# Optimization experiments

Measured on AMD Instinct MI355X. Metric: run time of the kernel, lower is better.

Reference implementation:

```python
import jax, jax.numpy as jnp
from jax import lax
import numpy as np


def setup_inputs() -> dict:
    key = jax.random.key(0)
    T, W = 2048, 30  # document length, max span width
    starts = jnp.repeat(jnp.arange(T, dtype=jnp.int32), W)      # [T*W]
    widths = jnp.tile(jnp.arange(W, dtype=jnp.int32), T)        # [T*W]
    ends = jnp.minimum(starts + widths, T - 1)
    spans = jnp.stack([starts, ends], axis=1)                   # [N,2], N=61440
    N = spans.shape[0]
    scores = jax.random.normal(key, (N,), dtype=jnp.float32)
    mask = jnp.ones((N,), dtype=jnp.float32)
    return {
        "spans": spans,
        "span_mention_scores": scores,
        "span_mask": mask,
        "token_num": T,
        "num_spans_to_keep": int(0.4 * T),
    }


def _greedy_non_crossing(spans, scores, mask, T, k):
    """Greedy NMS-style selection of up to k spans with no crossing overlap.
    Faithful to masked_topk_non_overlap: iterate candidates in descending
    (score + log(mask)) order; a candidate (s,e) is rejected iff it crosses
    an already-selected span, tracked via start_to_max_end / end_to_min_start
    tables. Sequential dependence expressed as lax.scan; the O(span_width)
    inner token loop is vectorized as an O(T) masked range query.
    """
    N = scores.shape[0]
    order = jnp.argsort(-(scores + jnp.log(mask)))  # descending sort
    starts = spans[:, 0].astype(jnp.int32)
    ends = spans[:, 1].astype(jnp.int32)
    tok = jnp.arange(T, dtype=jnp.int32)

    def step(carry, c):
        s2e, e2s, sel, cnt = carry
        s = starts[c]
        e = ends[c]
        # token_idx in (s, e] with start_to_max_end[token_idx] > e -> crossing
        cross1 = jnp.any((tok > s) & (tok <= e) & (s2e > e))
        # token_idx in [s, e) with 0 <= end_to_min_start[token_idx] < s -> crossing
        cross2 = jnp.any((tok >= s) & (tok < e) & (e2s >= 0) & (e2s < s))
        accept = jnp.logical_and(jnp.logical_not(cross1 | cross2), cnt < k)
        # start_to_max_end[s] = max(old, e) if accepted
        s2e = s2e.at[s].set(jnp.where(accept, jnp.maximum(s2e[s], e), s2e[s]))
        # end_to_min_start[e] = s if unset or s smaller, if accepted
        cur = e2s[e]
        e2s = e2s.at[e].set(jnp.where(accept & ((cur == -1) | (s < cur)), s, cur))
        sel = sel.at[c].set(sel[c] | accept)
        cnt = cnt + accept.astype(jnp.int32)
        return (s2e, e2s, sel, cnt), None

    init = (jnp.full((T,), -1, dtype=jnp.int32),
            jnp.full((T,), -1, dtype=jnp.int32),
            jnp.zeros((N,), dtype=bool),
            jnp.int32(0))
    (s2e, e2s, sel, cnt), _ = lax.scan(step, init, order)

    # sort selected candidates by (start, end); pad to fixed size k
    sort_key = jnp.where(sel, starts * T + ends, T * T)  # T*T > any valid key
    idx = jnp.argsort(sort_key)[:k]
    valid = jnp.arange(k) < cnt
    top_idx = jnp.where(valid, idx, 0)
    return top_idx, valid


def reference(spans, span_mention_scores, span_mask, token_num, num_spans_to_keep):
    top_idx, valid = _greedy_non_crossing(
        spans, span_mention_scores, span_mask, token_num, num_spans_to_keep)
    top_scores = jnp.where(valid, span_mention_scores[top_idx], 0.0)
    top_spans = jnp.where(valid[:, None], spans[top_idx], 0)
    return top_scores, top_idx, top_spans, valid
```

## Files before the change

kernel.cpp:

```cpp
#include <hip/hip_runtime.h>
#include <math.h>
#include <limits.h>

#define TPB   1024
#define TILE  1024
#define MAXT  2048
#define TPAD  64
#define MAXK  1024
#define MAXW  29
#define BATCH 1024
#define FLAGSTRIDE 16

struct SortSM {
  union {
    unsigned h[4 * 256];
    unsigned wcnt[16][256];
  };
  unsigned baseL[256];
};

__device__ inline void dbar(unsigned* flg, int nblk) {
  __syncthreads();
  if (threadIdx.x == 0) {
    __threadfence();
    atomicExch(&flg[blockIdx.x * FLAGSTRIDE], 1u);
  }
  if ((int)threadIdx.x < nblk) {
    int spin = 0;
    while (__hip_atomic_load(&flg[threadIdx.x * FLAGSTRIDE], __ATOMIC_ACQUIRE,
                             __HIP_MEMORY_SCOPE_AGENT) == 0u) {
      __builtin_amdgcn_s_sleep(2);
      if ((++spin & 255) == 0) {
        if (atomicAdd(&flg[threadIdx.x * FLAGSTRIDE], 0u) != 0u) break;
      }
    }
  }
  __syncthreads();
  if (threadIdx.x == 0) __threadfence();
  __syncthreads();
}

__device__ inline bool precheck30(const unsigned* tabP, int cc, int cs, int ce) {
  if (cc < 0) return false;
  int w = ce - cs;
  bool crossed = false;
  #pragma unroll
  for (int off = 0; off <= MAXW; ++off) {
    unsigned tv = tabP[cs + off];
    crossed |= ((off >= 1) & (off <= w) & ((tv & 0xFFFFu) > (unsigned)(ce + 1)))
             | ((off < w) & ((tv >> 16) < (unsigned)cs));
  }
  for (int off = MAXW + 1; off <= w; ++off) {
    unsigned tv = tabP[cs + off];
    crossed |= ((tv & 0xFFFFu) > (unsigned)(ce + 1));
    if (off < w) crossed |= ((tv >> 16) < (unsigned)cs);
  }
  return !crossed;
}

__global__ void __launch_bounds__(TPB, 4) fused_kernel(
    const int* __restrict__ spans, const float* __restrict__ scores,
    const float* __restrict__ mask, const int* __restrict__ tnum_p,
    const int* __restrict__ keep_p, float* __restrict__ out, int N, int nT,
    unsigned* pflag, unsigned* ghist, unsigned* tileCnt,
    unsigned* keysA, unsigned* keysB, int* idxA, int* idxB) {
  const int2* spans2 = (const int2*)spans;
  __shared__ SortSM s;
  __shared__ unsigned base4[4][256];
  const int tid = threadIdx.x;
  const int lane = tid & 63;
  const int wave = tid >> 6;

  if (tid < 1024) s.h[tid] = 0;
  __syncthreads();
  {
    int i = blockIdx.x * TILE + tid;
    if (i < N) {
      float kf = scores[i] + logf(mask[i]);
      unsigned u = __float_as_uint(kf);
      u = (u & 0x80000000u) ? ~u : (u | 0x80000000u);
      u = ~u;
      keysA[i] = u;
      atomicAdd(&s.h[(u & 255u)], 1u);
      atomicAdd(&s.h[256 + ((u >> 8) & 255u)], 1u);
      atomicAdd(&s.h[512 + ((u >> 16) & 255u)], 1u);
      atomicAdd(&s.h[768 + (u >> 24)], 1u);
    }
    __syncthreads();
    if (tid < 1024 && s.h[tid]) atomicAdd(&ghist[tid], s.h[tid]);
  }
  dbar(pflag + 0 * nT * FLAGSTRIDE, nT);

  if (wave < 4) {
    const int p = wave;
    unsigned v0 = ghist[p * 256 + 4 * lane + 0];
    unsigned v1 = ghist[p * 256 + 4 * lane + 1];
    unsigned v2 = ghist[p * 256 + 4 * lane + 2];
    unsigned v3 = ghist[p * 256 + 4 * lane + 3];
    unsigned sum = v0 + v1 + v2 + v3;
    unsigned x = sum;
    for (int off = 1; off < 64; off <<= 1) {
      unsigned y = __shfl_up(x, off, 64);
      if (lane >= off) x += y;
    }
    unsigned excl = x - sum;
    base4[p][4 * lane + 0] = excl;
    base4[p][4 * lane + 1] = excl + v0;
    base4[p][4 * lane + 2] = excl + v0 + v1;
    base4[p][4 * lane + 3] = excl + v0 + v1 + v2;
  }
  __syncthreads();

  for (int p = 0; p < 4; ++p) {
    const unsigned* srck = (p & 1) ? keysB : keysA;
    const int*      srci = (p & 1) ? idxB : idxA;
    unsigned*       dstk = (p & 1) ? keysA : keysB;
    int*            dsti = (p & 1) ? idxA : idxB;
    const int shift = 8 * p;
    unsigned* lbf = pflag + (1 + p) * nT * FLAGSTRIDE;

    for (int j = tid; j < 16 * 256; j += TPB)
      (&s.wcnt[0][0])[j] = 0;
    __syncthreads();

    int i = blockIdx.x * TILE + tid;
    bool v = (i < N);
    unsigned key = v ? srck[i] : 0u;
    int pay = v ? ((p == 0) ? i : srci[i]) : 0;
    unsigned d = (key >> shift) & 255u;
    unsigned long long mm = __ballot(v);
    #pragma unroll
    for (int b = 0; b < 8; ++b) {
      unsigned long long bb = __ballot((d >> b) & 1u);
      mm &= ((d >> b) & 1u) ? bb : ~bb;
    }
    unsigned rnk = (unsigned)__popcll(mm & ((1ull << lane) - 1ull));
    if (v && rnk == 0) s.wcnt[wave][d] = (unsigned)__popcll(mm);
    __syncthreads();
    if (tid < 256) {
      unsigned run = 0;
      #pragma unroll
      for (int g = 0; g < 16; ++g) {
        unsigned c = s.wcnt[g][tid];
        s.wcnt[g][tid] = run;
        run += c;
      }
      tileCnt[blockIdx.x * 256 + tid] = run;
    }
    __syncthreads();

    if (tid == 0) {
      __threadfence();
      atomicExch(&lbf[blockIdx.x * FLAGSTRIDE], 1u);
    }
    if (tid < blockIdx.x) {
      int spin = 0;
      while (__hip_atomic_load(&lbf[tid * FLAGSTRIDE], __ATOMIC_ACQUIRE,
                               __HIP_MEMORY_SCOPE_AGENT) == 0u) {
        __builtin_amdgcn_s_sleep(2);
        if ((++spin & 255) == 0) {
          if (atomicAdd(&lbf[tid * FLAGSTRIDE], 0u) != 0u) break;
        }
      }
    }
    __syncthreads();
    if (tid == 0) __threadfence();
    __syncthreads();

    if (tid < 256) {
      unsigned baseacc = base4[p][tid];
      for (int t = 0; t < blockIdx.x; ++t)
        baseacc += tileCnt[t * 256 + tid];
      s.baseL[tid] = baseacc;
    }
    __syncthreads();
    if (v) {
      unsigned pos = s.baseL[d] + s.wcnt[wave][d] + rnk;
      dstk[pos] = key;
      dsti[pos] = pay;
    }
    if (p < 3) {
      dbar(pflag + (5 + p) * nT * FLAGSTRIDE, nT);
    }
  }

  {
    unsigned* fin = pflag + 8 * nT * FLAGSTRIDE;
    __syncthreads();
    if (tid == 0) {
      __threadfence();
      atomicExch(&fin[blockIdx.x * FLAGSTRIDE], 1u);
    }
    if (blockIdx.x != 0) return;
    if (tid < nT) {
      int spin = 0;
      while (__hip_atomic_load(&fin[tid * FLAGSTRIDE], __ATOMIC_ACQUIRE,
                               __HIP_MEMORY_SCOPE_AGENT) == 0u) {
        __builtin_amdgcn_s_sleep(2);
        if ((++spin & 255) == 0) {
          if (atomicAdd(&fin[tid * FLAGSTRIDE], 0u) != 0u) break;
        }
      }
    }
    __syncthreads();
    if (tid == 0) __threadfence();
    __syncthreads();
  }

  const int* order = idxA;
  __shared__ unsigned tabP[MAXT + TPAD];
  __shared__ int2 tab[MAXT + TPAD];
  __shared__ unsigned long long acc[MAXK];
  __shared__ unsigned long long surv[BATCH];
  __shared__ unsigned long long Cmat[BATCH];
  __shared__ int wvs[16];
  __shared__ int gcnt;

  const int T  = tnum_p[0];
  const int k0 = keep_p[0];
  const int k  = (k0 < MAXK) ? k0 : MAXK;

  for (int t = tid; t < MAXT + TPAD; t += TPB) {
    tab[t] = make_int2(-1, INT_MAX);
    tabP[t] = 0xFFFF0000u;
  }
  if (tid == 0) gcnt = 0;
  __syncthreads();

  int cc = -1, cs = 0, ce = 0, nn = -1;
  if (tid < N)         cc = order[tid];
  if (BATCH + tid < N) nn = order[BATCH + tid];
  if (cc >= 0) { int2 sp = spans2[cc]; cs = sp.x; ce = sp.y; }

  int cnt = 0;
  for (int c0 = 0; c0 < N && cnt < k; c0 += BATCH) {
    int pc = nn, ps = 0, pe = 0;
    if (pc >= 0) { int2 sp = spans2[pc]; ps = sp.x; pe = sp.y; }
    int i2 = c0 + 2 * BATCH + tid;
    nn = (i2 < N) ? order[i2] : -1;

    bool ok = precheck30(tabP, cc, cs, ce);
    unsigned long long bal = __ballot(ok);
    if (lane == 0) wvs[wave] = (int)__popcll(bal);
    __syncthreads();
    int ns = 0, wb = 0;
    #pragma unroll
    for (int w2 = 0; w2 < 16; ++w2) {
      if (w2 == wave) wb = ns;
      ns += wvs[w2];
    }

    if (ns > 0) {
      if (ok) {
        int pos = wb + (int)__popcll(bal & ((1ull << lane) - 1ull));
        surv[pos] = ((unsigned long long)(unsigned)cs << 48)
                  | ((unsigned long long)(unsigned)ce << 32)
                  | (unsigned)cc;
      }
      __syncthreads();

      for (int v = tid; v < ns; v += TPB) {
        unsigned long long pk = surv[v];
        int gs = (int)(pk >> 48), ge = (int)((pk >> 32) & 0xFFFFu);
        int gbase = v & ~63;
        int m = ns - gbase; if (m > 64) m = 64;
        unsigned long long C = 0;
        for (int j = 0; j < m; ++j) {
          unsigned long long pj = surv[gbase + j];
          int sj = (int)(pj >> 48), ej = (int)((pj >> 32) & 0xFFFFu);
          bool cr = (gs < sj && sj <= ge && ej > ge) ||
                    (sj < gs && gs <= ej && ej < ge);
          C |= (unsigned long long)cr << j;
        }
        Cmat[v] = C;
      }
      __syncthreads();

      if (tid < 64) {
        bool dirty = false;
        for (int g = 0; g < ns && cnt < k; g += 64) {
          int m = ns - g; if (m > 64) m = 64;
          bool act = lane < m;
          int gs = 0, ge = 0, gc = 0;
          unsigned long long C = 0;
          if (act) {
            unsigned long long pk = surv[g + lane];
            gs = (int)(pk >> 48);
            ge = (int)((pk >> 32) & 0xFFFFu);
            gc = (int)(unsigned)pk;
            C  = Cmat[g + lane];
          }
          bool pre = act;
          if (dirty) {
            pre = act && precheck30(tabP, gc, gs, ge);
          }
          unsigned long long preB = __ballot(pre);
          if (preB == 0ull) continue;
          int np = (int)__popcll(preB);
          unsigned long long lower = (1ull << lane) - 1ull;
          unsigned long long accm;
          int cnt0g = cnt;
          if (np == 1) {
            accm = preB;
            cnt += 1;
          } else {
            unsigned long long Cl = C & lower;
            unsigned long long resolvedB = ~preB;
            accm = 0ull;
            while (true) {
              bool meUn   = ((resolvedB >> lane) & 1ull) == 0ull;
              bool killed = (Cl & accm) != 0ull;
              bool ready  = (Cl & ~resolvedB) == 0ull;
              unsigned long long newacc = __ballot(meUn && ready && !killed);
              unsigned long long newrej = __ballot(meUn && killed);
              if (!(newacc | newrej)) break;
              accm |= newacc;
              resolvedB |= (newacc | newrej);
            }
            int nacc = (int)__popcll(accm);
            if (cnt + nacc > k) {
              int room = k - cnt;
              bool a0 = ((accm >> lane) & 1ull) != 0ull;
              int ar = (int)__popcll(accm & lower);
              accm = __ballot(a0 && (ar < room));
              nacc = room;
            }
            cnt += nacc;
          }
          bool accme = ((accm >> lane) & 1ull) != 0ull;
          if (accme) {
            int rank = (int)__popcll(accm & lower);
            acc[cnt0g + rank] =
                ((unsigned long long)(unsigned)(gs * T + ge) << 32) | (unsigned)gc;
            atomicMax(&tab[gs].x, ge);
            atomicMin(&tab[ge].y, gs);
          }
          if (accme) {
            int2 tv = tab[gs];
            tabP[gs] = ((unsigned)(tv.y > 65535 ? 65535 : tv.y) << 16)
                     | (unsigned)(tv.x + 1);
            int2 tv2 = tab[ge];
            tabP[ge] = ((unsigned)(tv2.y > 65535 ? 65535 : tv2.y) << 16)
                     | (unsigned)(tv2.x + 1);
          }
          if (accm) dirty = true;
        }
        if (lane == 0) gcnt = cnt;
      }
      __syncthreads();
      cnt = gcnt;
    }

    cc = pc; cs = ps; ce = pe;
  }

  int M = 2;
  while (M < cnt) M <<= 1;
  for (int j = tid; j < M; j += TPB)
    if (j >= cnt) acc[j] = ~0ull;
  __syncthreads();
  for (int kk = 2; kk <= M; kk <<= 1) {
    for (int jj = kk >> 1; jj > 0; jj >>= 1) {
      for (int i3 = tid; i3 < M; i3 += TPB) {
        int ixj = i3 ^ jj;
        if (ixj > i3) {
          unsigned long long a = acc[i3], b = acc[ixj];
          bool up = ((i3 & kk) == 0);
          if ((a > b) == up) { acc[i3] = b; acc[ixj] = a; }
        }
      }
      __syncthreads();
    }
  }

  for (int j = tid; j < k0; j += TPB) {
    if (j < cnt) {
      int cand = (int)(acc[j] & 0xFFFFFFFFu);
      out[j]                  = scores[cand];
      out[k0 + j]             = (float)cand;
      out[2 * k0 + 2 * j]     = (float)spans[2 * cand];
      out[2 * k0 + 2 * j + 1] = (float)spans[2 * cand + 1];
      out[4 * k0 + j]         = 1.0f;
    } else {
      out[j]                  = 0.0f;
      out[k0 + j]             = 0.0f;
      out[2 * k0 + 2 * j]     = 0.0f;
      out[2 * k0 + 2 * j + 1] = 0.0f;
      out[4 * k0 + j]         = 0.0f;
    }
  }
}

extern "C" void kernel_launch(void* const* d_in, const int* in_sizes, int n_in,
                              void* d_out, int out_size, void* d_ws, size_t ws_size,
                              hipStream_t stream) {
  const int*   spans  = (const int*)d_in[0];
  const float* scores = (const float*)d_in[1];
  const float* mask   = (const float*)d_in[2];
  const int*   tnum   = (const int*)d_in[3];
  const int*   keep   = (const int*)d_in[4];
  const int N = in_sizes[1];
  const int nT = (N + TILE - 1) / TILE;

  unsigned* pflag   = (unsigned*)d_ws;
  unsigned* ghist   = pflag + (size_t)9 * nT * FLAGSTRIDE;
  unsigned* tileCnt = ghist + 1024;
  unsigned* keysA   = tileCnt + (size_t)nT * 256;
  unsigned* keysB   = keysA + N;
  int*      idxA    = (int*)(keysB + N);
  int*      idxB    = idxA + N;
  float*    out     = (float*)d_out;

  hipMemsetAsync(pflag, 0,
                 ((size_t)9 * nT * FLAGSTRIDE + 1024) * sizeof(unsigned),
                 stream);

  fused_kernel<<<nT, TPB, 0, stream>>>(spans, scores, mask, tnum, keep, out,
                                       N, nT, pflag, ghist, tileCnt,
                                       keysA, keysB, idxA, idxB);
}
```

Baseline: 245.9 us.

## Replace per-candidate crossing precheck with a per-start rejection bitmask table

Adds a shared-memory bitmask R indexed by span start, where bit w marks that the span (s, s+w) crosses some already-accepted span. After each batch, the newly accepted spans scatter their crossing masks into R with atomicOr. The per-candidate precheck then becomes a single bit lookup instead of the 30-token table scan. This trades a cheaper hot-path filter for an extra scatter pass and barrier per batch, and it assumes span widths stay within MAXW.

After: 253.7 us. +3.2%, slower.

```diff
diff --git a/kernel.cpp b/kernel.cpp
--- a/kernel.cpp
+++ b/kernel.cpp
@@ -210,7 +210,9 @@
   const int* order = idxA;
   __shared__ unsigned tabP[MAXT + TPAD];
   __shared__ int2 tab[MAXT + TPAD];
+  __shared__ unsigned R[MAXT];
   __shared__ unsigned long long acc[MAXK];
+  __shared__ unsigned racc_s[MAXK];
   __shared__ unsigned long long surv[BATCH];
   __shared__ unsigned long long Cmat[BATCH];
   __shared__ int wvs[16];
@@ -223,6 +225,7 @@
   for (int t = tid; t < MAXT + TPAD; t += TPB) {
     tab[t] = make_int2(-1, INT_MAX);
     tabP[t] = 0xFFFF0000u;
+    if (t < MAXT) R[t] = 0u;
   }
   if (tid == 0) gcnt = 0;
   __syncthreads();
@@ -239,7 +242,7 @@
     int i2 = c0 + 2 * BATCH + tid;
     nn = (i2 < N) ? order[i2] : -1;
 
-    bool ok = precheck30(tabP, cc, cs, ce);
+    bool ok = (cc >= 0) && !((R[cs] >> (unsigned)(ce - cs)) & 1u);
     unsigned long long bal = __ballot(ok);
     if (lane == 0) wvs[wave] = (int)__popcll(bal);
     __syncthreads();
@@ -276,6 +279,7 @@
       }
       __syncthreads();
 
+      const int cntPrev = cnt;
       if (tid < 64) {
         bool dirty = false;
         for (int g = 0; g < ns && cnt < k; g += 64) {
@@ -332,6 +336,7 @@
             int rank = (int)__popcll(accm & lower);
             acc[cnt0g + rank] =
                 ((unsigned long long)(unsigned)(gs * T + ge) << 32) | (unsigned)gc;
+            racc_s[cnt0g + rank] = ((unsigned)gs << 16) | (unsigned)ge;
             atomicMax(&tab[gs].x, ge);
             atomicMin(&tab[ge].y, gs);
           }
@@ -349,6 +354,33 @@
       }
       __syncthreads();
       cnt = gcnt;
+
+      {
+        int nacc = cnt - cntPrev;
+        for (int it = tid; it < nacc * 64; it += TPB) {
+          unsigned pr = racc_s[cntPrev + (it >> 6)];
+          int as = (int)(pr >> 16), ae = (int)(pr & 0xFFFFu);
+          if (ae > as) {
+            int sx = as - MAXW + (it & 63);
+            if (sx >= 0 && sx <= ae && sx != as) {
+              unsigned mmask = 0u;
+              if (sx < as) {
+                int l1 = as - sx;
+                int h1 = ae - 1 - sx; if (h1 > MAXW) h1 = MAXW;
+                if (h1 >= l1)
+                  mmask = ((1u << (h1 + 1)) - 1u) & ~((1u << l1) - 1u);
+              } else {
+                int l2 = ae - sx + 1;
+                int h2 = T - 1 - sx; if (h2 > MAXW) h2 = MAXW;
+                if (h2 >= l2)
+                  mmask = ((1u << (h2 + 1)) - 1u) & ~((1u << l2) - 1u);
+              }
+              if (mmask) atomicOr(&R[sx], mmask);
+            }
+          }
+        }
+      }
+      __syncthreads();
     }
 
     cc = pc; cs = ps; ce = pe;
```
